# Kernel optimization log

Measured on AMD Instinct MI355X. Metric: run time of the kernel, lower is better.

## Reference

```python
import jax, jax.numpy as jnp
import numpy as np
import math

L, B, S, D, H, R = 4, 2, 1024, 1024, 16, 4
DH = D // H
SCALE = 1.0 / math.sqrt(DH)
EPS = 1e-5  # torch LayerNorm default


def _xavier(key, shape):
    fan_in, fan_out = shape[-2], shape[-1]
    bound = math.sqrt(6.0 / (fan_in + fan_out))
    return jax.random.uniform(key, shape, minval=-bound, maxval=bound, dtype=jnp.float32)


def setup_inputs() -> dict:
    key = jax.random.key(0)
    ks = jax.random.split(key, 12)
    f32 = jnp.float32
    return {
        "x": jax.random.normal(ks[0], (B, S, D), f32),
        "sigma": jnp.full((L,), 0.1, f32),
        "U": jax.random.normal(ks[1], (L, D, R), f32),
        "V": jax.random.normal(ks[2], (L, R, D), f32),
        "Wqkv1": _xavier(ks[3], (L, D, 3 * D)),
        "Wqkv2": _xavier(ks[4], (L, D, 3 * D)),
        "Wp1": _xavier(ks[5], (L, D // 2, D)),
        "bp1": jnp.zeros((L, D), f32),
        "Wp2": _xavier(ks[6], (L, D // 2, D)),
        "bp2": jnp.zeros((L, D), f32),
        "Wo": _xavier(ks[7], (L, D, D)),
        "bo": jnp.zeros((L, D), f32),
        "g_out": jnp.ones((L, D), f32), "b_out": jnp.zeros((L, D), f32),
        "g1": jnp.ones((L, D), f32), "b1": jnp.zeros((L, D), f32),
        "g2": jnp.ones((L, D), f32), "b2": jnp.zeros((L, D), f32),
        "Wm1": _xavier(ks[8], (L, D, 4 * D)),
        "bm1": jnp.zeros((L, 4 * D), f32),
        "Wm2": _xavier(ks[9], (L, 4 * D, D)),
        "bm2": jnp.zeros((L, D), f32),
        "gf": jnp.ones((D,), f32), "bf": jnp.zeros((D,), f32),
    }


def _ln(h, g, b):
    m = h.mean(-1, keepdims=True)
    v = ((h - m) ** 2).mean(-1, keepdims=True)
    return (h - m) * jax.lax.rsqrt(v + EPS) * g + b


def _heads(t):  # [B,S,D] -> [B,H,S,DH]
    return t.reshape(B, S, H, DH).transpose(0, 2, 1, 3)


def _forward(x, sigma, U, V, Wqkv1, Wqkv2, Wp1, bp1, Wp2, bp2, Wo, bo,
             g_out, b_out, g1, b1, g2, b2, Wm1, bm1, Wm2, bm2, gf, bf):
    params = (sigma, U, V, Wqkv1, Wqkv2, Wp1, bp1, Wp2, bp2, Wo, bo,
              g_out, b_out, g1, b1, g2, b2, Wm1, bm1, Wm2, bm2)

    def layer(xc, p):
        (sig, U_, V_, Wq1, Wq2, Wp1_, bp1_, Wp2_, bp2_, Wo_, bo_,
         gO, bO, g1_, b1_, g2_, b2_, Wm1_, bm1_, Wm2_, bm2_) = p
        h = _ln(xc, g1_, b1_)
        # svd_adapt = (sigma * (U @ V)).sum(-1) broadcast over batch/seq
        adapt = (sig * (U_ @ V_)).sum(-1)  # [D]
        a = h + adapt
        x1, x2 = jnp.split(a, 2, axis=-1)
        x1 = x1 @ Wp1_ + bp1_
        x2 = x2 @ Wp2_ + bp2_
        q1, k1, v1 = jnp.split(x1 @ Wq1, 3, axis=-1)
        q2, k2, v2 = jnp.split(x2 @ Wq2, 3, axis=-1)
        q1, k1, v1, q2, k2, v2 = map(_heads, (q1, k1, v1, q2, k2, v2))
        a1 = jax.nn.softmax(jnp.einsum('bhqd,bhkd->bhqk', q1, k1) * SCALE, axis=-1)
        a2 = jax.nn.softmax(jnp.einsum('bhqd,bhkd->bhqk', q2, k2) * SCALE, axis=-1)
        diff = a1 - a2
        # (diff@v1 + diff@v2)/2 == diff @ ((v1+v2)/2)
        out = jnp.einsum('bhqk,bhkd->bhqd', diff, (v1 + v2) * 0.5)
        out = out.transpose(0, 2, 1, 3).reshape(B, S, D)
        out = _ln(out @ Wo_ + bo_, gO, bO)
        xc = xc + out
        h2 = _ln(xc, g2_, b2_)
        xc = xc + (jax.nn.gelu(h2 @ Wm1_ + bm1_, approximate=False) @ Wm2_ + bm2_)
        return xc, None

    x, _ = jax.lax.scan(layer, x, params)
    return _ln(x, gf, bf)


def reference(x, sigma, U, V, Wqkv1, Wqkv2, Wp1, bp1, Wp2, bp2, Wo, bo,
              g_out, b_out, g1, b1, g2, b2, Wm1, bm1, Wm2, bm2, gf, bf):
    return _forward(x, sigma, U, V, Wqkv1, Wqkv2, Wp1, bp1, Wp2, bp2, Wo, bo,
                    g_out, b_out, g1, b1, g2, b2, Wm1, bm1, Wm2, bm2, gf, bf)
```

## Files before the change

### kernel.cpp

```cpp
#include <hip/hip_runtime.h>
#include <math.h>

typedef unsigned short u16;
typedef short bf16x8 __attribute__((ext_vector_type(8)));
typedef float f32x4 __attribute__((ext_vector_type(4)));

__device__ __forceinline__ float bf2f(u16 u){ return __uint_as_float(((unsigned)u)<<16); }
__device__ __forceinline__ u16 f2bf(float f){
  unsigned u = __float_as_uint(f);
  u += 0x7fffu + ((u>>16)&1u);
  return (u16)(u>>16);
}
__device__ __forceinline__ float gelu_f(float x){ return 0.5f*x*(1.0f+erff(x*0.7071067811865476f)); }

__device__ __forceinline__ unsigned cvtpk_bf16(float a, float b){
  unsigned r; asm("v_cvt_pk_bf16_f32 %0, %1, %2" : "=v"(r) : "v"(a), "v"(b)); return r;
}

__device__ __forceinline__ void gload16(const void* g, void* l){
  __builtin_amdgcn_global_load_lds((const __attribute__((address_space(1))) void*)g,
                                   (__attribute__((address_space(3))) void*)l, 16, 0, 0);
}

__device__ __forceinline__ float block_sum(float v, float* sh){
  #pragma unroll
  for (int o=32;o;o>>=1) v += __shfl_down(v,o,64);
  int w = threadIdx.x>>6, lane = threadIdx.x&63;
  __syncthreads();
  if (lane==0) sh[w]=v;
  __syncthreads();
  return sh[0]+sh[1]+sh[2]+sh[3];
}

template<int FM,int FN,int OF32,int ACC,int ACT>
__global__ __launch_bounds__(256) void gemm2_k(
    const u16* __restrict__ A, const u16* __restrict__ Bm, void* __restrict__ Cv,
    const float* __restrict__ bias, int biasz,
    int K,int lda,int ldb,int ldc,float alpha,
    long sAz,long sBz,long sCz)
{
  constexpr int BM = FM*32, BN = FN*32;
  int zz = blockIdx.z;
  const u16* Ap = A  + (long)zz*sAz;
  const u16* Bp = Bm + (long)zz*sBz;
  long coff = (long)zz*sCz;
  int m0 = blockIdx.y*BM, n0 = blockIdx.x*BN;
  __shared__ __align__(16) u16 As[BM][64];
  __shared__ __align__(16) u16 Bs[BN][64];
  u16* AsF = &As[0][0]; u16* BsF = &Bs[0][0];
  int tid = threadIdx.x, w = tid>>6, l = tid&63;
  int q = l>>4, m16 = l&15;
  int wr = w>>1, wc = w&1;
  int sr  = w*8 + (l>>3);
  int sch = (l&7) ^ ((l>>3)&7);
  int s7  = m16 & 7;

  f32x4 acc[FM][FN];
  #pragma unroll
  for (int i=0;i<FM;i++)
    #pragma unroll
    for (int j=0;j<FN;j++) acc[i][j] = (f32x4){0.f,0.f,0.f,0.f};

  int aRow = wr*(FM*16) + m16;
  int bRow = wc*(FN*16) + m16;

  for (int k0=0;k0<K;k0+=64){
    __syncthreads();
    #pragma unroll
    for (int c=0;c<FM;c++)
      gload16(Ap + (long)(m0 + c*32 + sr)*lda + k0 + sch*8, AsF + c*2048 + w*512);
    #pragma unroll
    for (int c=0;c<FN;c++)
      gload16(Bp + (long)(n0 + c*32 + sr)*ldb + k0 + sch*8, BsF + c*2048 + w*512);
    __syncthreads();
    #pragma unroll
    for (int kh=0;kh<2;kh++){
      bf16x8 afr[FM], bfr[FN];
      #pragma unroll
      for (int i=0;i<FM;i++)
        afr[i] = *(const bf16x8*)(AsF + (aRow + i*16)*64 + (((kh<<2)|q) ^ s7)*8);
      #pragma unroll
      for (int j=0;j<FN;j++)
        bfr[j] = *(const bf16x8*)(BsF + (bRow + j*16)*64 + (((kh<<2)|q) ^ s7)*8);
      #pragma unroll
      for (int i=0;i<FM;i++)
        #pragma unroll
        for (int j=0;j<FN;j++)
          acc[i][j] = __builtin_amdgcn_mfma_f32_16x16x32_bf16(afr[i], bfr[j], acc[i][j], 0,0,0);
    }
  }
  #pragma unroll
  for (int j=0;j<FN;j++){
    int n = n0 + wc*(FN*16) + j*16 + m16;
    float bv = bias ? bias[(long)zz*biasz + n] : 0.0f;
    #pragma unroll
    for (int i=0;i<FM;i++){
      #pragma unroll
      for (int r=0;r<4;r++){
        int m = m0 + wr*(FM*16) + i*16 + q*4 + r;
        float v = acc[i][j][r]*alpha + bv;
        if (ACT==1) v = gelu_f(v);
        long ci = coff + (long)m*ldc + n;
        if (OF32){
          float* C = (float*)Cv;
          if (ACC) C[ci] += v; else C[ci] = v;
        } else {
          ((u16*)Cv)[ci] = f2bf(v);
        }
      }
    }
  }
}

__device__ __forceinline__ void flash_stream(
    const u16* Kl, const u16* Vl, u16* Plw,
    bf16x8 qa, bf16x8 qb, int qd, int m16,
    float& mrun, float& lsum, f32x4* O)
{
  int r7 = m16 & 7;
  f32x4 s[4];
  __builtin_amdgcn_s_setprio(1);
  #pragma unroll
  for (int f=0;f<4;f++){
    s[f] = (f32x4){0.f,0.f,0.f,0.f};
    int row = f*16 + m16;
    bf16x8 ka = *(const bf16x8*)(Kl + row*64 + ((qd    ) ^ r7)*8);
    bf16x8 kb = *(const bf16x8*)(Kl + row*64 + ((4 + qd) ^ r7)*8);
    s[f] = __builtin_amdgcn_mfma_f32_16x16x32_bf16(ka, qa, s[f], 0,0,0);
    s[f] = __builtin_amdgcn_mfma_f32_16x16x32_bf16(kb, qb, s[f], 0,0,0);
  }
  __builtin_amdgcn_s_setprio(0);
  const float SC2 = 0.18033688011112042f;
  float sc[16]; float pmax = -1e30f;
  #pragma unroll
  for (int f=0;f<4;f++)
    #pragma unroll
    for (int r=0;r<4;r++){ float v = s[f][r]*SC2; sc[f*4+r]=v; pmax = fmaxf(pmax,v); }
  pmax = fmaxf(pmax, __shfl_xor(pmax,16,64));
  pmax = fmaxf(pmax, __shfl_xor(pmax,32,64));
  bool resc = __any(pmax - mrun > 12.0f);
  float mnew = resc ? fmaxf(mrun, pmax) : mrun;
  float psum = 0.f;
  #pragma unroll
  for (int f=0;f<4;f++){
    float e0 = exp2f(sc[f*4+0]-mnew), e1 = exp2f(sc[f*4+1]-mnew);
    float e2 = exp2f(sc[f*4+2]-mnew), e3 = exp2f(sc[f*4+3]-mnew);
    psum += (e0+e1)+(e2+e3);
    uint2 pv; pv.x = cvtpk_bf16(e0,e1); pv.y = cvtpk_bf16(e2,e3);
    *(uint2*)(Plw + m16*72 + f*16 + qd*4) = pv;
  }
  psum += __shfl_xor(psum,16,64);
  psum += __shfl_xor(psum,32,64);
  if (resc){
    float corr = exp2f(mrun - mnew);
    lsum = lsum*corr + psum;
    mrun = mnew;
    float cO[4];
    #pragma unroll
    for (int r=0;r<4;r++) cO[r] = __shfl(corr, qd*4 + r, 64);
    #pragma unroll
    for (int f2=0;f2<4;f2++)
      #pragma unroll
      for (int r=0;r<4;r++) O[f2][r] *= cO[r];
  } else {
    lsum += psum;
  }
  __builtin_amdgcn_s_setprio(1);
  #pragma unroll
  for (int b32=0;b32<2;b32++){
    bf16x8 pa = *(const bf16x8*)(Plw + m16*72 + b32*32 + qd*8);
    #pragma unroll
    for (int f2=0;f2<4;f2++){
      int row = f2*16 + m16;
      bf16x8 vb = *(const bf16x8*)(Vl + row*64 + (((b32<<2)|qd) ^ r7)*8);
      O[f2] = __builtin_amdgcn_mfma_f32_16x16x32_bf16(pa, vb, O[f2], 0,0,0);
    }
  }
  __builtin_amdgcn_s_setprio(0);
}

__global__ __launch_bounds__(256) void flash_k(
    const u16* __restrict__ qkv1, const u16* __restrict__ qkv2,
    const u16* __restrict__ vavgC, u16* __restrict__ outp)
{
  __shared__ __align__(16) u16 K1l[4096];
  __shared__ __align__(16) u16 K2l[4096];
  __shared__ __align__(16) u16 Vl[4096];
  __shared__ __align__(16) u16 Pl[4608];
  int z = blockIdx.y, b = z>>4, h = z&15;
  int q0 = blockIdx.x*64;
  int tid = threadIdx.x, w = tid>>6, l = tid&63;
  int qd = l>>4, m16 = l&15;
  int lr = l>>3;
  int sch = (l&7) ^ lr;
  u16* Plw = Pl + w*1152;

  const u16* q1p = qkv1 + ((long)(b*1024 + q0 + w*16 + m16))*2048 + h*64;
  const u16* q2p = qkv2 + ((long)(b*1024 + q0 + w*16 + m16))*2048 + h*64;
  bf16x8 q1a = *(const bf16x8*)(q1p + qd*8);
  bf16x8 q1b = *(const bf16x8*)(q1p + 32 + qd*8);
  bf16x8 q2a = *(const bf16x8*)(q2p + qd*8);
  bf16x8 q2b = *(const bf16x8*)(q2p + 32 + qd*8);

  const u16* k1base = qkv1 + ((long)(b*1024))*2048 + 1024 + h*64;
  const u16* k2base = qkv2 + ((long)(b*1024))*2048 + 1024 + h*64;
  const u16* vbase  = vavgC + (long)(h*64)*2048 + b*1024;

  float m1 = -1e30f, l1 = 0.f, m2 = -1e30f, l2 = 0.f;
  f32x4 O1[4], O2[4];
  #pragma unroll
  for (int f=0;f<4;f++){ O1[f]=(f32x4){0.f,0.f,0.f,0.f}; O2[f]=(f32x4){0.f,0.f,0.f,0.f}; }

  for (int t=0;t<16;t++){
    __syncthreads();
    #pragma unroll
    for (int c2=0;c2<2;c2++){
      int r = c2*32 + w*8 + lr;
      gload16(k1base + (long)(t*64 + r)*2048 + sch*8, K1l + c2*2048 + w*512);
      gload16(k2base + (long)(t*64 + r)*2048 + sch*8, K2l + c2*2048 + w*512);
      gload16(vbase  + (long)r*2048 + t*64 + sch*8,   Vl  + c2*2048 + w*512);
    }
    __syncthreads();
    flash_stream(K1l, Vl, Plw, q1a, q1b, qd, m16, m1, l1, O1);
    flash_stream(K2l, Vl, Plw, q2a, q2b, qd, m16, m2, l2, O2);
  }
  float inv1 = 1.0f/l1, inv2 = 1.0f/l2;
  float i1O[4], i2O[4];
  #pragma unroll
  for (int r=0;r<4;r++){ i1O[r] = __shfl(inv1, qd*4+r, 64); i2O[r] = __shfl(inv2, qd*4+r, 64); }
  #pragma unroll
  for (int f2=0;f2<4;f2++){
    #pragma unroll
    for (int r=0;r<4;r++){
      long idx = ((long)(b*1024 + q0 + w*16 + qd*4 + r))*1024 + h*64 + f2*16 + m16;
      outp[idx] = f2bf(O1[f2][r]*i1O[r] - O2[f2][r]*i2O[r]);
    }
  }
}

__global__ __launch_bounds__(256) void wtc_k(
    const float* __restrict__ in0, const float* __restrict__ in1,
    u16* __restrict__ out0, u16* __restrict__ out1,
    int stride, int ldout, int koff0, int koff1){
  const float* in = blockIdx.z ? in1 : in0;
  u16* out = blockIdx.z ? out1 : out0;
  int koff = blockIdx.z ? koff1 : koff0;
  __shared__ float tile[64][65];
  int bx = blockIdx.x, by = blockIdx.y;
  int t = threadIdx.x, r = t>>6, c = t&63;
  const float* ip = in + (long)(by*64)*stride + bx*64;
  #pragma unroll
  for (int i=0;i<16;i++) tile[i*4+r][c] = ip[(long)(i*4+r)*stride + c];
  __syncthreads();
  u16* op = out + (long)(bx*64)*ldout + by*64 + koff;
  #pragma unroll
  for (int i=0;i<16;i++) op[(long)(i*4+r)*ldout + c] = f2bf(tile[c][i*4+r]);
}

template<int ACCXC,int HAS_OUT,int OUTF32>
__global__ __launch_bounds__(256) void ln_k(const float* __restrict__ in,
    const float* __restrict__ g, const float* __restrict__ b,
    float* __restrict__ xc, void* __restrict__ out)
{
  __shared__ float sh[4];
  long row = blockIdx.x;
  int tid = threadIdx.x;
  float x[4];
  #pragma unroll
  for (int i=0;i<4;i++) x[i] = in[row*1024 + tid + 256*i];
  float s = x[0]+x[1]+x[2]+x[3];
  float mean = block_sum(s, sh) * (1.0f/1024.0f);
  float ss = 0.f;
  #pragma unroll
  for (int i=0;i<4;i++){ float d = x[i]-mean; ss += d*d; }
  float var = block_sum(ss, sh) * (1.0f/1024.0f);
  float rstd = rsqrtf(var + 1e-5f);
  #pragma unroll
  for (int i=0;i<4;i++){
    int col = tid + 256*i;
    long idx = row*1024 + col;
    float val = (x[i]-mean)*rstd*g[col];
    if (b) val += b[col];
    if (ACCXC) xc[idx] += val;
    if (HAS_OUT){
      if (OUTF32) ((float*)out)[idx] = val;
      else ((u16*)out)[idx] = f2bf(val);
    }
  }
}

__global__ void cvt_k(const float* __restrict__ x, float* __restrict__ xc){
  long i = (long)blockIdx.x*256 + threadIdx.x;
  xc[i] = x[i];
}

__global__ void abar_k(const float* __restrict__ sig, const float* __restrict__ U,
                       const float* __restrict__ V, const float* __restrict__ b1,
                       float* __restrict__ abar){
  __shared__ float vs[4];
  int tid = threadIdx.x, w = tid>>6, lane = tid&63;
  float p = 0.f;
  #pragma unroll
  for (int i=0;i<16;i++) p += V[w*1024 + lane + 64*i];
  #pragma unroll
  for (int o=32;o;o>>=1) p += __shfl_down(p,o,64);
  if (lane==0) vs[w] = p;
  __syncthreads();
  float sg = sig[0];
  for (int d=tid; d<1024; d+=256){
    float a = 0.f;
    #pragma unroll
    for (int r=0;r<4;r++) a += U[d*4+r]*vs[r];
    abar[d] = b1[d] + sg*a;
  }
}

__global__ void bar1p_k(const float* __restrict__ abar,
                        const float* __restrict__ Wp1, const float* __restrict__ Wp2,
                        float* __restrict__ bp){
  int n = blockIdx.x*256 + threadIdx.x;
  int kc = blockIdx.y;
  float s1=0.f, s2=0.f;
  for (int j=0;j<32;j++){
    int k = kc*32+j;
    s1 += abar[k]     * Wp1[(long)k*1024 + n];
    s2 += abar[512+k] * Wp2[(long)k*1024 + n];
  }
  bp[kc*2048 + n] = s1; bp[kc*2048 + 1024 + n] = s2;
}
__global__ void bar1r_k(const float* __restrict__ bp,
                        const float* __restrict__ bp1, const float* __restrict__ bp2,
                        float* __restrict__ x1bar, float* __restrict__ x2bar){
  int n = blockIdx.x*256 + threadIdx.x;
  float s1 = bp1[n], s2 = bp2[n];
  for (int kc=0;kc<16;kc++){ s1 += bp[kc*2048+n]; s2 += bp[kc*2048+1024+n]; }
  x1bar[n] = s1; x2bar[n] = s2;
}
__global__ void bar2p_k(const float* __restrict__ x1bar, const float* __restrict__ x2bar,
                        const float* __restrict__ Wq1, const float* __restrict__ Wq2,
                        float* __restrict__ qp){
  int n = blockIdx.x*256 + threadIdx.x;
  int kc = blockIdx.y;
  float s1 = 0.f, s2 = 0.f;
  for (int j=0;j<32;j++){
    int k = kc*32+j;
    s1 += x1bar[k] * Wq1[(long)k*3072 + n];
    s2 += x2bar[k] * Wq2[(long)k*3072 + n];
  }
  qp[kc*1024 + n] = s1; qp[32768 + kc*1024 + n] = s2;
}
__global__ void bar2r_k(const float* __restrict__ qp, float* __restrict__ qbias){
  int m = blockIdx.x*256 + threadIdx.x;
  int st = m>>11, n = m&2047;
  float s = 0.f;
  if (n < 1024){ for (int kc=0;kc<32;kc++) s += qp[st*32768 + kc*1024 + n]; }
  qbias[m] = s;
}

extern "C" void kernel_launch(void* const* d_in, const int* in_sizes, int n_in,
                              void* d_out, int out_size, void* d_ws, size_t ws_size,
                              hipStream_t stream){
  const float* X    = (const float*)d_in[0];
  const float* SIG  = (const float*)d_in[1];
  const float* U    = (const float*)d_in[2];
  const float* V    = (const float*)d_in[3];
  const float* Wqkv1= (const float*)d_in[4];
  const float* Wqkv2= (const float*)d_in[5];
  const float* Wp1  = (const float*)d_in[6];
  const float* bp1  = (const float*)d_in[7];
  const float* Wp2  = (const float*)d_in[8];
  const float* bp2  = (const float*)d_in[9];
  const float* Wo   = (const float*)d_in[10];
  const float* bo   = (const float*)d_in[11];
  const float* gO   = (const float*)d_in[12];
  const float* bO   = (const float*)d_in[13];
  const float* g1   = (const float*)d_in[14];
  const float* b1   = (const float*)d_in[15];
  const float* g2   = (const float*)d_in[16];
  const float* b2   = (const float*)d_in[17];
  const float* Wm1  = (const float*)d_in[18];
  const float* bm1  = (const float*)d_in[19];
  const float* Wm2  = (const float*)d_in[20];
  const float* bm2  = (const float*)d_in[21];
  const float* gf   = (const float*)d_in[22];
  const float* bfv  = (const float*)d_in[23];
  (void)in_sizes; (void)n_in; (void)out_size; (void)ws_size;

  const long MB = 1024*1024;
  char* p = (char*)d_ws;
  float* xc    = (float*)(p);
  u16* qkv1    = (u16*)(p + 8*MB);
  u16* qkv2    = (u16*)(p + 16*MB);
  u16* bufA    = (u16*)(p + 24*MB);
  u16* x12w    = (u16*)(p + 28*MB);
  u16* vavgC   = (u16*)(p + 36*MB);
  float* bp    = (float*)(p + 36*MB);
  float* qp    = (float*)(p + 36*MB + 131072);
  u16* wpT1    = (u16*)(p + 40*MB);
  u16* wqkvT1  = (u16*)(p + 42*MB);
  u16* wqkvT2  = (u16*)(p + 46*MB);
  u16* wvT12   = (u16*)(p + 50*MB);
  u16* mid     = (u16*)(p + 40*MB);
  float* projout=(float*)(p + 56*MB);
  float* qbias = (float*)(p + 56*MB);
  u16* woT     = (u16*)(p + 8*MB);
  u16* wm1T    = (u16*)(p + 10*MB);
  u16* wm2T    = (u16*)(p + 28*MB);
  float* abar  = (float*)(p + 64*MB);
  float* x1bar = (float*)(p + 64*MB + 4096);
  float* x2bar = (float*)(p + 64*MB + 8192);

  u16* a_bf = bufA; u16* attnout = bufA; u16* h2 = bufA;
  u16* wpT2 = wpT1 + 524288;

  cvt_k<<<8192,256,0,stream>>>(X, xc);
  for (int l=0;l<4;l++){
    const float* Wqkv1l = Wqkv1+(long)l*3145728;
    const float* Wqkv2l = Wqkv2+(long)l*3145728;
    abar_k<<<1,256,0,stream>>>(SIG+l, U+(long)l*4096, V+(long)l*4096, b1+l*1024, abar);
    bar1p_k<<<dim3(4,16),256,0,stream>>>(abar, Wp1+(long)l*524288, Wp2+(long)l*524288, bp);
    bar1r_k<<<4,256,0,stream>>>(bp, bp1+l*1024, bp2+l*1024, x1bar, x2bar);
    bar2p_k<<<dim3(4,32),256,0,stream>>>(x1bar, x2bar, Wqkv1l, Wqkv2l, qp);
    bar2r_k<<<16,256,0,stream>>>(qp, qbias);
    wtc_k<<<dim3(16,8,2), 256,0,stream>>>(Wp1+(long)l*524288, Wp2+(long)l*524288,
                                          wpT1, wpT2, 1024, 512, 0, 0);
    wtc_k<<<dim3(32,16,2),256,0,stream>>>(Wqkv1l, Wqkv2l, wqkvT1, wqkvT2, 3072, 1024, 0, 0);
    wtc_k<<<dim3(16,16,2),256,0,stream>>>(Wqkv1l+2048, Wqkv2l+2048, wvT12, wvT12, 3072, 2048, 0, 1024);
    ln_k<0,1,0><<<2048,256,0,stream>>>(xc, g1+l*1024, nullptr, nullptr, a_bf);
    gemm2_k<4,4,0,0,0><<<dim3(8,16,2),256,0,stream>>>(a_bf, wpT1, x12w, nullptr, 0,
        512, 1024, 512, 2048, 1.0f, 512, 524288, 1024);
    gemm2_k<4,4,0,0,0><<<dim3(16,16,2),256,0,stream>>>(x12w, wqkvT1, qkv1, qbias, 2048,
        1024, 2048, 1024, 2048, 1.0f, 1024, 2097152, 4194304);
    gemm2_k<4,4,0,0,0><<<dim3(16,8,1),256,0,stream>>>(wvT12, x12w, vavgC, nullptr, 0,
        2048, 2048, 2048, 2048, 0.5f, 0, 0, 0);
    flash_k<<<dim3(16,32),256,0,stream>>>(qkv1, qkv2, vavgC, attnout);
    wtc_k<<<dim3(16,16,1),256,0,stream>>>(Wo +(long)l*1048576, nullptr, woT,  nullptr, 1024, 1024, 0, 0);
    wtc_k<<<dim3(64,16,1),256,0,stream>>>(Wm1+(long)l*4194304, nullptr, wm1T, nullptr, 4096, 1024, 0, 0);
    wtc_k<<<dim3(16,64,1),256,0,stream>>>(Wm2+(long)l*4194304, nullptr, wm2T, nullptr, 1024, 4096, 0, 0);
    gemm2_k<2,4,1,0,0><<<dim3(8,32,1),256,0,stream>>>(attnout, woT, projout, bo+l*1024, 0,
        1024, 1024, 1024, 1024, 1.0f, 0, 0, 0);
    ln_k<1,0,0><<<2048,256,0,stream>>>(projout, gO+l*1024, bO+l*1024, xc, nullptr);
    ln_k<0,1,0><<<2048,256,0,stream>>>(xc, g2+l*1024, b2+l*1024, nullptr, h2);
    gemm2_k<4,4,0,0,1><<<dim3(32,16,1),256,0,stream>>>(h2, wm1T, mid, bm1+l*4096, 0,
        1024, 1024, 1024, 4096, 1.0f, 0, 0, 0);
    gemm2_k<2,4,1,1,0><<<dim3(8,32,1),256,0,stream>>>(mid, wm2T, (void*)xc, bm2+l*1024, 0,
        4096, 4096, 4096, 1024, 1.0f, 0, 0, 0);
  }
  ln_k<0,1,1><<<2048,256,0,stream>>>(xc, gf, bfv, nullptr, (float*)d_out);
}
```

Baseline: 1.514 ms.

## Double-buffer GEMM and flash LDS tiles, swizzle blocks, shrink tiles, split-K MLP2

The GEMM and flash-attention kernels now double-buffer their LDS tiles, so the next K/V or A/B tile is fetched while MFMAs run on the current one, with one barrier per iteration. Block indices are remapped across eight groups to change how blocks are spread and improve cache locality. Most GEMM launches use smaller tiles and more blocks to raise occupancy. The final MLP GEMM uses split-K over two z-slices that accumulate with atomicAdd, adding bias only from slice zero. The cost is twice the LDS per block, which may lower occupancy, plus atomic traffic and a summation order that can vary between runs.

```diff
diff --git a/kernel.cpp b/kernel.cpp
--- a/kernel.cpp
+++ b/kernel.cpp
@@ -44,10 +44,12 @@
   const u16* Ap = A  + (long)zz*sAz;
   const u16* Bp = Bm + (long)zz*sBz;
   long coff = (long)zz*sCz;
-  int m0 = blockIdx.y*BM, n0 = blockIdx.x*BN;
-  __shared__ __align__(16) u16 As[BM][64];
-  __shared__ __align__(16) u16 Bs[BN][64];
-  u16* AsF = &As[0][0]; u16* BsF = &Bs[0][0];
+  unsigned nx = gridDim.x, orig = blockIdx.y*nx + blockIdx.x;
+  unsigned cpx = (nx*gridDim.y)>>3;
+  unsigned swz = (orig&7u)*cpx + (orig>>3);
+  int m0 = (int)(swz/nx)*BM, n0 = (int)(swz%nx)*BN;
+  __shared__ __align__(16) u16 As[2][BM][64];
+  __shared__ __align__(16) u16 Bs[2][BN][64];
   int tid = threadIdx.x, w = tid>>6, l = tid&63;
   int q = l>>4, m16 = l&15;
   int wr = w>>1, wc = w&1;
@@ -63,16 +65,26 @@
 
   int aRow = wr*(FM*16) + m16;
   int bRow = wc*(FN*16) + m16;
-
-  for (int k0=0;k0<K;k0+=64){
-    __syncthreads();
+  int nt = K>>6;
+
+  auto STAGE = [&](int t, int buf){
+    int k0 = t<<6;
     #pragma unroll
     for (int c=0;c<FM;c++)
-      gload16(Ap + (long)(m0 + c*32 + sr)*lda + k0 + sch*8, AsF + c*2048 + w*512);
+      gload16(Ap + (long)(m0 + c*32 + sr)*lda + k0 + sch*8, &As[buf][c*32][0] + w*512);
     #pragma unroll
     for (int c=0;c<FN;c++)
-      gload16(Bp + (long)(n0 + c*32 + sr)*ldb + k0 + sch*8, BsF + c*2048 + w*512);
-    __syncthreads();
+      gload16(Bp + (long)(n0 + c*32 + sr)*ldb + k0 + sch*8, &Bs[buf][c*32][0] + w*512);
+  };
+
+  STAGE(0, 0);
+  __syncthreads();
+  for (int t=0;t<nt;t++){
+    int buf = t&1;
+    if (t+1<nt) STAGE(t+1, buf^1);
+    const u16* AsF = &As[buf][0][0];
+    const u16* BsF = &Bs[buf][0][0];
+    __builtin_amdgcn_s_setprio(1);
     #pragma unroll
     for (int kh=0;kh<2;kh++){
       bf16x8 afr[FM], bfr[FN];
@@ -88,11 +100,14 @@
         for (int j=0;j<FN;j++)
           acc[i][j] = __builtin_amdgcn_mfma_f32_16x16x32_bf16(afr[i], bfr[j], acc[i][j], 0,0,0);
     }
+    __builtin_amdgcn_s_setprio(0);
+    __syncthreads();
   }
   #pragma unroll
   for (int j=0;j<FN;j++){
     int n = n0 + wc*(FN*16) + j*16 + m16;
-    float bv = bias ? bias[(long)zz*biasz + n] : 0.0f;
+    float bv = 0.0f;
+    if (bias && (ACC!=2 || zz==0)) bv = bias[(long)zz*biasz + n];
     #pragma unroll
     for (int i=0;i<FM;i++){
       #pragma unroll
@@ -103,7 +118,9 @@
         long ci = coff + (long)m*ldc + n;
         if (OF32){
           float* C = (float*)Cv;
-          if (ACC) C[ci] += v; else C[ci] = v;
+          if (ACC==1) C[ci] += v;
+          else if (ACC==2) atomicAdd(&C[ci], v);
+          else C[ci] = v;
         } else {
           ((u16*)Cv)[ci] = f2bf(v);
         }
@@ -183,12 +200,13 @@
     const u16* __restrict__ qkv1, const u16* __restrict__ qkv2,
     const u16* __restrict__ vavgC, u16* __restrict__ outp)
 {
-  __shared__ __align__(16) u16 K1l[4096];
-  __shared__ __align__(16) u16 K2l[4096];
-  __shared__ __align__(16) u16 Vl[4096];
+  __shared__ __align__(16) u16 KV[2][3][4096];
   __shared__ __align__(16) u16 Pl[4608];
-  int z = blockIdx.y, b = z>>4, h = z&15;
-  int q0 = blockIdx.x*64;
+  unsigned nx = gridDim.x, orig = blockIdx.y*nx + blockIdx.x;
+  unsigned cpx = (nx*gridDim.y)>>3;
+  unsigned swz = (orig&7u)*cpx + (orig>>3);
+  int z = (int)(swz/nx), b = z>>4, h = z&15;
+  int q0 = (int)(swz%nx)*64;
   int tid = threadIdx.x, w = tid>>6, l = tid&63;
   int qd = l>>4, m16 = l&15;
   int lr = l>>3;
@@ -211,18 +229,24 @@
   #pragma unroll
   for (int f=0;f<4;f++){ O1[f]=(f32x4){0.f,0.f,0.f,0.f}; O2[f]=(f32x4){0.f,0.f,0.f,0.f}; }
 
-  for (int t=0;t<16;t++){
-    __syncthreads();
+  auto STAGE = [&](int t, int buf){
     #pragma unroll
     for (int c2=0;c2<2;c2++){
       int r = c2*32 + w*8 + lr;
-      gload16(k1base + (long)(t*64 + r)*2048 + sch*8, K1l + c2*2048 + w*512);
-      gload16(k2base + (long)(t*64 + r)*2048 + sch*8, K2l + c2*2048 + w*512);
-      gload16(vbase  + (long)r*2048 + t*64 + sch*8,   Vl  + c2*2048 + w*512);
-    }
+      gload16(k1base + (long)(t*64 + r)*2048 + sch*8, &KV[buf][0][c2*2048 + w*512]);
+      gload16(k2base + (long)(t*64 + r)*2048 + sch*8, &KV[buf][1][c2*2048 + w*512]);
+      gload16(vbase  + (long)r*2048 + t*64 + sch*8,   &KV[buf][2][c2*2048 + w*512]);
+    }
+  };
+
+  STAGE(0, 0);
+  __syncthreads();
+  for (int t=0;t<16;t++){
+    int buf = t&1;
+    if (t<15) STAGE(t+1, buf^1);
+    flash_stream(&KV[buf][0][0], &KV[buf][2][0], Plw, q1a, q1b, qd, m16, m1, l1, O1);
+    flash_stream(&KV[buf][1][0], &KV[buf][2][0], Plw, q2a, q2b, qd, m16, m2, l2, O2);
     __syncthreads();
-    flash_stream(K1l, Vl, Plw, q1a, q1b, qd, m16, m1, l1, O1);
-    flash_stream(K2l, Vl, Plw, q2a, q2b, qd, m16, m2, l2, O2);
   }
   float inv1 = 1.0f/l1, inv2 = 1.0f/l2;
   float i1O[4], i2O[4];
@@ -427,24 +451,24 @@
     wtc_k<<<dim3(32,16,2),256,0,stream>>>(Wqkv1l, Wqkv2l, wqkvT1, wqkvT2, 3072, 1024, 0, 0);
     wtc_k<<<dim3(16,16,2),256,0,stream>>>(Wqkv1l+2048, Wqkv2l+2048, wvT12, wvT12, 3072, 2048, 0, 1024);
     ln_k<0,1,0><<<2048,256,0,stream>>>(xc, g1+l*1024, nullptr, nullptr, a_bf);
-    gemm2_k<4,4,0,0,0><<<dim3(8,16,2),256,0,stream>>>(a_bf, wpT1, x12w, nullptr, 0,
+    gemm2_k<2,4,0,0,0><<<dim3(8,32,2),256,0,stream>>>(a_bf, wpT1, x12w, nullptr, 0,
         512, 1024, 512, 2048, 1.0f, 512, 524288, 1024);
-    gemm2_k<4,4,0,0,0><<<dim3(16,16,2),256,0,stream>>>(x12w, wqkvT1, qkv1, qbias, 2048,
+    gemm2_k<2,4,0,0,0><<<dim3(16,32,2),256,0,stream>>>(x12w, wqkvT1, qkv1, qbias, 2048,
         1024, 2048, 1024, 2048, 1.0f, 1024, 2097152, 4194304);
-    gemm2_k<4,4,0,0,0><<<dim3(16,8,1),256,0,stream>>>(wvT12, x12w, vavgC, nullptr, 0,
+    gemm2_k<2,2,0,0,0><<<dim3(32,16,1),256,0,stream>>>(wvT12, x12w, vavgC, nullptr, 0,
         2048, 2048, 2048, 2048, 0.5f, 0, 0, 0);
     flash_k<<<dim3(16,32),256,0,stream>>>(qkv1, qkv2, vavgC, attnout);
     wtc_k<<<dim3(16,16,1),256,0,stream>>>(Wo +(long)l*1048576, nullptr, woT,  nullptr, 1024, 1024, 0, 0);
     wtc_k<<<dim3(64,16,1),256,0,stream>>>(Wm1+(long)l*4194304, nullptr, wm1T, nullptr, 4096, 1024, 0, 0);
     wtc_k<<<dim3(16,64,1),256,0,stream>>>(Wm2+(long)l*4194304, nullptr, wm2T, nullptr, 1024, 4096, 0, 0);
-    gemm2_k<2,4,1,0,0><<<dim3(8,32,1),256,0,stream>>>(attnout, woT, projout, bo+l*1024, 0,
+    gemm2_k<2,2,1,0,0><<<dim3(16,32,1),256,0,stream>>>(attnout, woT, projout, bo+l*1024, 0,
         1024, 1024, 1024, 1024, 1.0f, 0, 0, 0);
     ln_k<1,0,0><<<2048,256,0,stream>>>(projout, gO+l*1024, bO+l*1024, xc, nullptr);
     ln_k<0,1,0><<<2048,256,0,stream>>>(xc, g2+l*1024, b2+l*1024, nullptr, h2);
-    gemm2_k<4,4,0,0,1><<<dim3(32,16,1),256,0,stream>>>(h2, wm1T, mid, bm1+l*4096, 0,
+    gemm2_k<2,4,0,0,1><<<dim3(32,32,1),256,0,stream>>>(h2, wm1T, mid, bm1+l*4096, 0,
         1024, 1024, 1024, 4096, 1.0f, 0, 0, 0);
-    gemm2_k<2,4,1,1,0><<<dim3(8,32,1),256,0,stream>>>(mid, wm2T, (void*)xc, bm2+l*1024, 0,
-        4096, 4096, 4096, 1024, 1.0f, 0, 0, 0);
+    gemm2_k<2,4,1,2,0><<<dim3(8,32,2),256,0,stream>>>(mid, wm2T, (void*)xc, bm2+l*1024, 0,
+        2048, 4096, 4096, 1024, 1.0f, 2048, 2048, 0);
   }
   ln_k<0,1,1><<<2048,256,0,stream>>>(xc, gf, bfv, nullptr, (float*)d_out);
 }
```

Result: faster. 1.379 ms (-8.9%).
